# Performance work log

Hardware: AMD Instinct MI355X
Metric: run time of the kernel (lower is better)

## Reference

```python
import jax, jax.numpy as jnp
import numpy as np

N, H, E = 50000, 128, 1600000

def setup_inputs() -> dict:
    key = jax.random.key(0)
    k1, k2, k3, k4 = jax.random.split(key, 4)
    h = jax.random.normal(k1, (N, H), dtype=jnp.float32)
    edge_index = jax.random.randint(k2, (2, E), 0, N, dtype=jnp.int64)
    # edge_scorer: Linear(2H, 1); node_scorer: Linear(H, 1)
    W_edge = jax.random.normal(k3, (2 * H, 1), dtype=jnp.float32) / np.sqrt(2 * H)
    b_edge = jnp.zeros((1,), dtype=jnp.float32)
    W_node = jax.random.normal(k4, (H, 1), dtype=jnp.float32) / np.sqrt(H)
    b_node = jnp.zeros((1,), dtype=jnp.float32)
    return {"h": h, "edge_index": edge_index, "W_edge": W_edge,
            "b_edge": b_edge, "W_node": W_node, "b_node": b_node}

def reference(h, edge_index, W_edge, b_edge, W_node, b_node):
    n = h.shape[0]
    src, dst = edge_index[0], edge_index[1]
    # cat([h[src], h[dst]]) @ W_edge == (h @ W_src)[src] + (h @ W_dst)[dst]
    # (same math as the torch module, avoids materializing the (E, 2H) concat)
    W_src, W_dst = W_edge[:h.shape[1]], W_edge[h.shape[1]:]
    s_src = (h @ W_src)[:, 0]            # (N,)
    s_dst = (h @ W_dst)[:, 0]            # (N,)
    edge_scores = s_src[src] + s_dst[dst] + b_edge[0]   # (E,)
    node_edge_score = jax.ops.segment_sum(edge_scores, dst, num_segments=n)
    node_self_score = (h @ W_node)[:, 0] + b_node[0]    # (N,)
    combined = node_edge_score + node_self_score
    return jax.nn.softmax(combined, axis=0)
```

## Files before the change

kernel.cpp:

```cpp
#include <hip/hip_runtime.h>
#include <math.h>


#define RANGE_BITS 14
#define RANGE_SIZE (1 << RANGE_BITS)
#define NCHUNKS 64
#define STAT_BLOCKS 256

typedef float vfloat4 __attribute__((ext_vector_type(4)));

__global__ __launch_bounds__(256) void node_scores_kernel(
    const float* __restrict__ h,
    const float* __restrict__ W_edge,
    const float* __restrict__ b_edge,
    const float* __restrict__ W_node,
    const float* __restrict__ b_node,
    float* __restrict__ s_src,
    float* __restrict__ t_dst,
    float* __restrict__ self_sc,
    float* __restrict__ acc,
    int N, int H)
{
    const int lane16 = threadIdx.x & 15;
    const int n = (blockIdx.x * blockDim.x + threadIdx.x) >> 4;
    if (n >= N) return;

    const float4* __restrict__ h4  = (const float4*)(h + (size_t)n * H);
    const float4* __restrict__ ws4 = (const float4*)(W_edge);
    const float4* __restrict__ wd4 = (const float4*)(W_edge + H);
    const float4* __restrict__ wn4 = (const float4*)(W_node);
    const int H4 = H >> 2;

    float ps = 0.0f, pd = 0.0f, pn = 0.0f;
    for (int i = lane16; i < H4; i += 16) {
        float4 hv = h4[i];
        float4 a = ws4[i], b = wd4[i], c = wn4[i];
        ps = fmaf(hv.x, a.x, fmaf(hv.y, a.y, fmaf(hv.z, a.z, fmaf(hv.w, a.w, ps))));
        pd = fmaf(hv.x, b.x, fmaf(hv.y, b.y, fmaf(hv.z, b.z, fmaf(hv.w, b.w, pd))));
        pn = fmaf(hv.x, c.x, fmaf(hv.y, c.y, fmaf(hv.z, c.z, fmaf(hv.w, c.w, pn))));
    }
    #pragma unroll
    for (int off = 8; off > 0; off >>= 1) {
        ps += __shfl_xor(ps, off, 64);
        pd += __shfl_xor(pd, off, 64);
        pn += __shfl_xor(pn, off, 64);
    }
    if (lane16 == 0) {
        float self = pn + b_node[0];
        s_src[n]   = ps;
        t_dst[n]   = pd + b_edge[0];
        self_sc[n] = self;
        acc[n]     = self;
    }
}

__global__ __launch_bounds__(1024) void edge_bin_swz_kernel(
    const int* __restrict__ ei,
    const float* __restrict__ s_src,
    const float* __restrict__ t_dst,
    float* __restrict__ partials,
    int N, int E, int chunk, int vec_ok)
{
    __shared__ float hist[RANGE_SIZE];
    const int id = blockIdx.x;
    const int g  = id & 7;
    const int s  = id >> 3;
    const int b  = (g << 3) | (s & 7);
    const int r  = s >> 3;
    const int lo = r << RANGE_BITS;
    const int hi = min(lo + RANGE_SIZE, N);
    const unsigned span = (unsigned)(hi - lo);

    {
        vfloat4* __restrict__ hz = (vfloat4*)hist;
        const vfloat4 z = {0.0f, 0.0f, 0.0f, 0.0f};
        for (int i = threadIdx.x; i < (RANGE_SIZE >> 2); i += blockDim.x)
            hz[i] = z;
    }
    __syncthreads();

    const int e0 = b * chunk;
    const int e1 = min(e0 + chunk, E);
    if (e0 < e1) {
        if (vec_ok) {
            const int nvec = (e1 - e0) >> 2;
            const int4* __restrict__ dst4 = (const int4*)(ei + E + e0);
            const int4* __restrict__ src4 = (const int4*)(ei + e0);
            int i = threadIdx.x;
            for (; i + (int)blockDim.x < nvec; i += 2 * blockDim.x) {
                int4 da = dst4[i];
                int4 db = dst4[i + blockDim.x];
                int4 sa = src4[i];
                int4 sb = src4[i + blockDim.x];
                unsigned ax = (unsigned)(da.x - lo), ay = (unsigned)(da.y - lo);
                unsigned az = (unsigned)(da.z - lo), aw = (unsigned)(da.w - lo);
                if (ax < span) atomicAdd(&hist[ax], s_src[sa.x] + t_dst[da.x]);
                if (ay < span) atomicAdd(&hist[ay], s_src[sa.y] + t_dst[da.y]);
                if (az < span) atomicAdd(&hist[az], s_src[sa.z] + t_dst[da.z]);
                if (aw < span) atomicAdd(&hist[aw], s_src[sa.w] + t_dst[da.w]);
                unsigned bx = (unsigned)(db.x - lo), by = (unsigned)(db.y - lo);
                unsigned bz = (unsigned)(db.z - lo), bw = (unsigned)(db.w - lo);
                if (bx < span) atomicAdd(&hist[bx], s_src[sb.x] + t_dst[db.x]);
                if (by < span) atomicAdd(&hist[by], s_src[sb.y] + t_dst[db.y]);
                if (bz < span) atomicAdd(&hist[bz], s_src[sb.z] + t_dst[db.z]);
                if (bw < span) atomicAdd(&hist[bw], s_src[sb.w] + t_dst[db.w]);
            }
            if (i < nvec) {
                int4 da = dst4[i];
                int4 sa = src4[i];
                unsigned ax = (unsigned)(da.x - lo), ay = (unsigned)(da.y - lo);
                unsigned az = (unsigned)(da.z - lo), aw = (unsigned)(da.w - lo);
                if (ax < span) atomicAdd(&hist[ax], s_src[sa.x] + t_dst[da.x]);
                if (ay < span) atomicAdd(&hist[ay], s_src[sa.y] + t_dst[da.y]);
                if (az < span) atomicAdd(&hist[az], s_src[sa.z] + t_dst[da.z]);
                if (aw < span) atomicAdd(&hist[aw], s_src[sa.w] + t_dst[da.w]);
            }
            for (int e = e0 + 4 * nvec + threadIdx.x; e < e1; e += blockDim.x) {
                int d = ei[E + e];
                unsigned u = (unsigned)(d - lo);
                if (u < span) atomicAdd(&hist[u], s_src[ei[e]] + t_dst[d]);
            }
        } else {
            for (int e = e0 + threadIdx.x; e < e1; e += blockDim.x) {
                int d = ei[E + e];
                unsigned u = (unsigned)(d - lo);
                if (u < span) atomicAdd(&hist[u], s_src[ei[e]] + t_dst[d]);
            }
        }
    }
    __syncthreads();

    float* __restrict__ outp = partials + (size_t)b * N + lo;
    const int len = hi - lo;
    if ((len & 3) == 0) {
        const int len4 = len >> 2;
        const vfloat4* __restrict__ h4 = (const vfloat4*)hist;
        vfloat4* __restrict__ o4 = (vfloat4*)outp;
        for (int i = threadIdx.x; i < len4; i += blockDim.x) o4[i] = h4[i];
    } else {
        for (int i = threadIdx.x; i < len; i += blockDim.x) outp[i] = hist[i];
    }
}

__global__ __launch_bounds__(1024) void edge_bin_kernel(
    const int* __restrict__ ei,
    const float* __restrict__ s_src,
    const float* __restrict__ t_dst,
    float* __restrict__ partials,
    int N, int E, int chunk, int vec_ok)
{
    __shared__ float hist[RANGE_SIZE];
    const int b  = blockIdx.x;
    const int r  = blockIdx.y;
    const int lo = r << RANGE_BITS;
    const int hi = min(lo + RANGE_SIZE, N);
    const unsigned span = (unsigned)(hi - lo);

    for (int i = threadIdx.x; i < RANGE_SIZE; i += blockDim.x) hist[i] = 0.0f;
    __syncthreads();

    const int e0 = b * chunk;
    const int e1 = min(e0 + chunk, E);
    if (e0 < e1) {
        if (vec_ok) {
            const int nvec = (e1 - e0) >> 2;
            const int4* __restrict__ dst4 = (const int4*)(ei + E + e0);
            const int4* __restrict__ src4 = (const int4*)(ei + e0);
            for (int i = threadIdx.x; i < nvec; i += blockDim.x) {
                int4 d = dst4[i];
                int4 s = src4[i];
                unsigned ux = (unsigned)(d.x - lo), uy = (unsigned)(d.y - lo);
                unsigned uz = (unsigned)(d.z - lo), uw = (unsigned)(d.w - lo);
                if (ux < span) atomicAdd(&hist[ux], s_src[s.x] + t_dst[d.x]);
                if (uy < span) atomicAdd(&hist[uy], s_src[s.y] + t_dst[d.y]);
                if (uz < span) atomicAdd(&hist[uz], s_src[s.z] + t_dst[d.z]);
                if (uw < span) atomicAdd(&hist[uw], s_src[s.w] + t_dst[d.w]);
            }
            for (int e = e0 + 4 * nvec + threadIdx.x; e < e1; e += blockDim.x) {
                int d = ei[E + e];
                unsigned u = (unsigned)(d - lo);
                if (u < span) atomicAdd(&hist[u], s_src[ei[e]] + t_dst[d]);
            }
        } else {
            for (int e = e0 + threadIdx.x; e < e1; e += blockDim.x) {
                int d = ei[E + e];
                unsigned u = (unsigned)(d - lo);
                if (u < span) atomicAdd(&hist[u], s_src[ei[e]] + t_dst[d]);
            }
        }
    }
    __syncthreads();

    float* __restrict__ outp = partials + (size_t)b * N + lo;
    const int len = hi - lo;
    for (int i = threadIdx.x; i < len; i += blockDim.x) outp[i] = hist[i];
}

__global__ __launch_bounds__(256) void edge_accum_fallback_kernel(
    const int* __restrict__ ei,
    const float* __restrict__ s_src,
    const float* __restrict__ t_dst,
    float* __restrict__ acc,
    int E)
{
    int e = blockIdx.x * blockDim.x + threadIdx.x;
    if (e >= E) return;
    int s = ei[e];
    int d = ei[E + e];
    atomicAdd(&acc[d], s_src[s] + t_dst[d]);
}

__device__ __forceinline__ float blockReduceMaxB(float v) {
    __shared__ float sm[16];
    #pragma unroll
    for (int off = 32; off > 0; off >>= 1) v = fmaxf(v, __shfl_xor(v, off, 64));
    const int w = threadIdx.x >> 6, l = threadIdx.x & 63;
    const int nw = blockDim.x >> 6;
    if (l == 0) sm[w] = v;
    __syncthreads();
    float r = sm[0];
    for (int i = 1; i < nw; ++i) r = fmaxf(r, sm[i]);
    __syncthreads();
    return r;
}

__device__ __forceinline__ float blockReduceSumB(float v) {
    __shared__ float sm[16];
    #pragma unroll
    for (int off = 32; off > 0; off >>= 1) v += __shfl_xor(v, off, 64);
    const int w = threadIdx.x >> 6, l = threadIdx.x & 63;
    const int nw = blockDim.x >> 6;
    if (l == 0) sm[w] = v;
    __syncthreads();
    float r = 0.0f;
    for (int i = 0; i < nw; ++i) r += sm[i];
    __syncthreads();
    return r;
}

__global__ __launch_bounds__(256) void combine_stats_kernel(
    const float* __restrict__ self_sc,
    const float* __restrict__ partials,
    float* __restrict__ acc,
    float* __restrict__ red,
    int N, int B, int use_partials)
{
    float m = -INFINITY, l = 0.0f;
    for (int i = blockIdx.x * blockDim.x + threadIdx.x; i < N;
         i += gridDim.x * blockDim.x) {
        float v;
        if (use_partials) {
            float v0 = self_sc[i], v1 = 0.0f, v2 = 0.0f, v3 = 0.0f;
            int b = 0;
            for (; b + 4 <= B; b += 4) {
                v0 += partials[(size_t)(b + 0) * N + i];
                v1 += partials[(size_t)(b + 1) * N + i];
                v2 += partials[(size_t)(b + 2) * N + i];
                v3 += partials[(size_t)(b + 3) * N + i];
            }
            for (; b < B; ++b) v0 += partials[(size_t)b * N + i];
            v = (v0 + v1) + (v2 + v3);
            acc[i] = v;
        } else {
            v = acc[i];
        }
        float nm = fmaxf(m, v);
        l = l * __expf(m - nm) + __expf(v - nm);
        m = nm;
    }
    float mb = blockReduceMaxB(m);
    float ladj = (m == -INFINITY) ? 0.0f : l * __expf(m - mb);
    float lb = blockReduceSumB(ladj);
    if (threadIdx.x == 0) {
        red[blockIdx.x] = mb;
        red[STAT_BLOCKS + blockIdx.x] = lb;
    }
}

__global__ __launch_bounds__(256) void finalize_kernel(
    const float* __restrict__ acc,
    const float* __restrict__ red,
    float* __restrict__ out,
    int N)
{
    float m = red[threadIdx.x];
    float l = red[STAT_BLOCKS + threadIdx.x];
    float M = blockReduceMaxB(m);
    float L = blockReduceSumB(l * __expf(m - M));
    const float inv = 1.0f / L;

    int i = blockIdx.x * blockDim.x + threadIdx.x;
    if (i < N) out[i] = __expf(acc[i] - M) * inv;
}

extern "C" void kernel_launch(void* const* d_in, const int* in_sizes, int n_in,
                              void* d_out, int out_size, void* d_ws, size_t ws_size,
                              hipStream_t stream) {
    const float* h      = (const float*)d_in[0];
    const int*   ei     = (const int*)  d_in[1];
    const float* W_edge = (const float*)d_in[2];
    const float* b_edge = (const float*)d_in[3];
    const float* W_node = (const float*)d_in[4];
    const float* b_node = (const float*)d_in[5];

    const int H = in_sizes[2] / 2;
    const int N = in_sizes[0] / H;
    const int E = in_sizes[1] / 2;

    float* out      = (float*)d_out;
    float* ws       = (float*)d_ws;
    float* s_src    = ws;
    float* t_dst    = ws + (size_t)N;
    float* self_s   = ws + 2 * (size_t)N;
    float* acc      = ws + 3 * (size_t)N;
    float* red      = ws + 4 * (size_t)N;
    float* partials = red + 2 * STAT_BLOCKS;

    const size_t base_floats = 4 * (size_t)N + 2 * STAT_BLOCKS;
    int B = 0;
    if (ws_size / sizeof(float) > base_floats) {
        size_t avail = ws_size / sizeof(float) - base_floats;
        B = (int)(avail / (size_t)N);
    }
    if (B > NCHUNKS) B = NCHUNKS;
    const int R = (N + RANGE_SIZE - 1) >> RANGE_BITS;
    const int use_partials = (B >= 16) ? 1 : 0;

    {
        int threads = N * 16;
        int grid = (threads + 255) / 256;
        node_scores_kernel<<<grid, 256, 0, stream>>>(
            h, W_edge, b_edge, W_node, b_node,
            s_src, t_dst, self_s, acc, N, H);
    }
    if (use_partials) {
        int chunk = (((E + B - 1) / B) + 3) & ~3;
        int vec_ok = ((E & 3) == 0) ? 1 : 0;
        if (B == NCHUNKS && R == 4) {
            edge_bin_swz_kernel<<<256, 1024, 0, stream>>>(
                ei, s_src, t_dst, partials, N, E, chunk, vec_ok);
        } else {
            dim3 grid(B, R);
            edge_bin_kernel<<<grid, 1024, 0, stream>>>(
                ei, s_src, t_dst, partials, N, E, chunk, vec_ok);
        }
    } else {
        int grid = (E + 255) / 256;
        edge_accum_fallback_kernel<<<grid, 256, 0, stream>>>(ei, s_src, t_dst, acc, E);
    }
    combine_stats_kernel<<<STAT_BLOCKS, 256, 0, stream>>>(
        self_s, partials, acc, red, N, B, use_partials);
    {
        int grid = (N + 255) / 256;
        finalize_kernel<<<grid, 256, 0, stream>>>(acc, red, out, N);
    }
}
```

Measured before the change: 112.7 us.

## Replace per-edge t_dst gather with LDS in-degree count applied at flush

Adds an edge binning kernel that keeps a per-node count histogram beside the sum histogram in LDS. The t_dst term is then applied once per node as count*t_dst at write-out instead of being gathered for every edge. This removes one random global gather per edge at the cost of a second LDS atomic per edge and double the LDS footprint (128 KB), which needs an opt-in shared memory attribute set through host queries on every call. The inner loop is also unrolled by two int4 loads, and the generic edge_bin_kernel is simplified to its scalar path.

```diff
diff --git a/kernel.cpp b/kernel.cpp
--- a/kernel.cpp
+++ b/kernel.cpp
@@ -8,6 +8,7 @@
 #define STAT_BLOCKS 256
 
 typedef float vfloat4 __attribute__((ext_vector_type(4)));
+typedef unsigned vuint4 __attribute__((ext_vector_type(4)));
 
 __global__ __launch_bounds__(256) void node_scores_kernel(
     const float* __restrict__ h,
@@ -51,6 +52,98 @@
         t_dst[n]   = pd + b_edge[0];
         self_sc[n] = self;
         acc[n]     = self;
+    }
+}
+
+__global__ __launch_bounds__(1024) void edge_bin_cnt_kernel(
+    const int* __restrict__ ei,
+    const float* __restrict__ s_src,
+    const float* __restrict__ t_dst,
+    float* __restrict__ partials,
+    int N, int E, int chunk, int vec_ok)
+{
+    extern __shared__ char smem_raw[];
+    float*    __restrict__ hsum = (float*)smem_raw;
+    unsigned* __restrict__ hcnt = (unsigned*)(smem_raw + (RANGE_SIZE << 2));
+
+    const int id = blockIdx.x;
+    const int g  = id & 7;
+    const int s  = id >> 3;
+    const int b  = (g << 3) | (s & 7);
+    const int r  = s >> 3;
+    const int lo = r << RANGE_BITS;
+    const int hi = min(lo + RANGE_SIZE, N);
+    const unsigned span = (unsigned)(hi - lo);
+
+    {
+        vfloat4* __restrict__ hz = (vfloat4*)hsum;
+        vuint4*  __restrict__ cz = (vuint4*)hcnt;
+        const vfloat4 zf = {0.0f, 0.0f, 0.0f, 0.0f};
+        const vuint4  zu = {0u, 0u, 0u, 0u};
+        for (int i = threadIdx.x; i < (RANGE_SIZE >> 2); i += blockDim.x) {
+            hz[i] = zf;
+            cz[i] = zu;
+        }
+    }
+    __syncthreads();
+
+    const int e0 = b * chunk;
+    const int e1 = min(e0 + chunk, E);
+    if (e0 < e1) {
+        if (vec_ok) {
+            const int nvec = (e1 - e0) >> 2;
+            const int4* __restrict__ dst4 = (const int4*)(ei + E + e0);
+            const int4* __restrict__ src4 = (const int4*)(ei + e0);
+            int i = threadIdx.x;
+            for (; i + (int)blockDim.x < nvec; i += 2 * blockDim.x) {
+                int4 da = dst4[i];
+                int4 db = dst4[i + blockDim.x];
+                int4 sa = src4[i];
+                int4 sb = src4[i + blockDim.x];
+                unsigned ax = (unsigned)(da.x - lo), ay = (unsigned)(da.y - lo);
+                unsigned az = (unsigned)(da.z - lo), aw = (unsigned)(da.w - lo);
+                if (ax < span) { atomicAdd(&hsum[ax], s_src[sa.x]); atomicAdd(&hcnt[ax], 1u); }
+                if (ay < span) { atomicAdd(&hsum[ay], s_src[sa.y]); atomicAdd(&hcnt[ay], 1u); }
+                if (az < span) { atomicAdd(&hsum[az], s_src[sa.z]); atomicAdd(&hcnt[az], 1u); }
+                if (aw < span) { atomicAdd(&hsum[aw], s_src[sa.w]); atomicAdd(&hcnt[aw], 1u); }
+                unsigned bx = (unsigned)(db.x - lo), by = (unsigned)(db.y - lo);
+                unsigned bz = (unsigned)(db.z - lo), bw = (unsigned)(db.w - lo);
+                if (bx < span) { atomicAdd(&hsum[bx], s_src[sb.x]); atomicAdd(&hcnt[bx], 1u); }
+                if (by < span) { atomicAdd(&hsum[by], s_src[sb.y]); atomicAdd(&hcnt[by], 1u); }
+                if (bz < span) { atomicAdd(&hsum[bz], s_src[sb.z]); atomicAdd(&hcnt[bz], 1u); }
+                if (bw < span) { atomicAdd(&hsum[bw], s_src[sb.w]); atomicAdd(&hcnt[bw], 1u); }
+            }
+            if (i < nvec) {
+                int4 da = dst4[i];
+                int4 sa = src4[i];
+                unsigned ax = (unsigned)(da.x - lo), ay = (unsigned)(da.y - lo);
+                unsigned az = (unsigned)(da.z - lo), aw = (unsigned)(da.w - lo);
+                if (ax < span) { atomicAdd(&hsum[ax], s_src[sa.x]); atomicAdd(&hcnt[ax], 1u); }
+                if (ay < span) { atomicAdd(&hsum[ay], s_src[sa.y]); atomicAdd(&hcnt[ay], 1u); }
+                if (az < span) { atomicAdd(&hsum[az], s_src[sa.z]); atomicAdd(&hcnt[az], 1u); }
+                if (aw < span) { atomicAdd(&hsum[aw], s_src[sa.w]); atomicAdd(&hcnt[aw], 1u); }
+            }
+            for (int e = e0 + 4 * nvec + threadIdx.x; e < e1; e += blockDim.x) {
+                int d = ei[E + e];
+                unsigned u = (unsigned)(d - lo);
+                if (u < span) { atomicAdd(&hsum[u], s_src[ei[e]]); atomicAdd(&hcnt[u], 1u); }
+            }
+        } else {
+            for (int e = e0 + threadIdx.x; e < e1; e += blockDim.x) {
+                int d = ei[E + e];
+                unsigned u = (unsigned)(d - lo);
+                if (u < span) { atomicAdd(&hsum[u], s_src[ei[e]]); atomicAdd(&hcnt[u], 1u); }
+            }
+        }
+    }
+    __syncthreads();
+
+    float* __restrict__ outp = partials + (size_t)b * N + lo;
+    const float* __restrict__ td = t_dst + lo;
+    const int len = hi - lo;
+    for (int i = threadIdx.x; i < len; i += blockDim.x) {
+        unsigned c = hcnt[i];
+        outp[i] = fmaf(__uint2float_rn(c), td[i], hsum[i]);
     }
 }
 
@@ -161,33 +254,10 @@
 
     const int e0 = b * chunk;
     const int e1 = min(e0 + chunk, E);
-    if (e0 < e1) {
-        if (vec_ok) {
-            const int nvec = (e1 - e0) >> 2;
-            const int4* __restrict__ dst4 = (const int4*)(ei + E + e0);
-            const int4* __restrict__ src4 = (const int4*)(ei + e0);
-            for (int i = threadIdx.x; i < nvec; i += blockDim.x) {
-                int4 d = dst4[i];
-                int4 s = src4[i];
-                unsigned ux = (unsigned)(d.x - lo), uy = (unsigned)(d.y - lo);
-                unsigned uz = (unsigned)(d.z - lo), uw = (unsigned)(d.w - lo);
-                if (ux < span) atomicAdd(&hist[ux], s_src[s.x] + t_dst[d.x]);
-                if (uy < span) atomicAdd(&hist[uy], s_src[s.y] + t_dst[d.y]);
-                if (uz < span) atomicAdd(&hist[uz], s_src[s.z] + t_dst[d.z]);
-                if (uw < span) atomicAdd(&hist[uw], s_src[s.w] + t_dst[d.w]);
-            }
-            for (int e = e0 + 4 * nvec + threadIdx.x; e < e1; e += blockDim.x) {
-                int d = ei[E + e];
-                unsigned u = (unsigned)(d - lo);
-                if (u < span) atomicAdd(&hist[u], s_src[ei[e]] + t_dst[d]);
-            }
-        } else {
-            for (int e = e0 + threadIdx.x; e < e1; e += blockDim.x) {
-                int d = ei[E + e];
-                unsigned u = (unsigned)(d - lo);
-                if (u < span) atomicAdd(&hist[u], s_src[ei[e]] + t_dst[d]);
-            }
-        }
+    for (int e = e0 + threadIdx.x; e < e1; e += blockDim.x) {
+        int d = ei[E + e];
+        unsigned u = (unsigned)(d - lo);
+        if (u < span) atomicAdd(&hist[u], s_src[ei[e]] + t_dst[d]);
     }
     __syncthreads();
 
@@ -326,6 +396,19 @@
     const int R = (N + RANGE_SIZE - 1) >> RANGE_BITS;
     const int use_partials = (B >= 16) ? 1 : 0;
 
+    const int want_lds = (RANGE_SIZE << 2) * 2;
+    int dev = 0;
+    hipGetDevice(&dev);
+    int optin = 0, maxsh = 0;
+    hipDeviceGetAttribute(&optin, hipDeviceAttributeSharedMemPerBlockOptin, dev);
+    hipDeviceGetAttribute(&maxsh, hipDeviceAttributeMaxSharedMemoryPerBlock, dev);
+    int use_cnt = (optin >= want_lds || maxsh >= want_lds) ? 1 : 0;
+    if (use_cnt) {
+        use_cnt = (hipFuncSetAttribute((const void*)edge_bin_cnt_kernel,
+                                       hipFuncAttributeMaxDynamicSharedMemorySize,
+                                       want_lds) == hipSuccess) ? 1 : 0;
+    }
+
     {
         int threads = N * 16;
         int grid = (threads + 255) / 256;
@@ -337,8 +420,13 @@
         int chunk = (((E + B - 1) / B) + 3) & ~3;
         int vec_ok = ((E & 3) == 0) ? 1 : 0;
         if (B == NCHUNKS && R == 4) {
-            edge_bin_swz_kernel<<<256, 1024, 0, stream>>>(
-                ei, s_src, t_dst, partials, N, E, chunk, vec_ok);
+            if (use_cnt) {
+                edge_bin_cnt_kernel<<<256, 1024, want_lds, stream>>>(
+                    ei, s_src, t_dst, partials, N, E, chunk, vec_ok);
+            } else {
+                edge_bin_swz_kernel<<<256, 1024, 0, stream>>>(
+                    ei, s_src, t_dst, partials, N, E, chunk, vec_ok);
+            }
         } else {
             dim3 grid(B, R);
             edge_bin_kernel<<<grid, 1024, 0, stream>>>(
```

Result: slower. 115.4 us (+2.4%).
